# Performance work log

Hardware: AMD Instinct MI355X
Metric: run time of the kernel (lower is better)

## Reference

```python
import jax, jax.numpy as jnp
import numpy as np

N = 20000   # nodes
E = 320000  # edges (avg degree 16)
K = 3       # Chebyshev order


def _glorot(key, shape):
    fan_in, fan_out = shape[-2], shape[-1]
    lim = (6.0 / (fan_in + fan_out)) ** 0.5
    return jax.random.uniform(key, shape, minval=-lim, maxval=lim, dtype=jnp.float32)


def setup_inputs() -> dict:
    key = jax.random.key(0)
    ks = jax.random.split(key, 8)
    v = jax.random.normal(ks[0], (N, 86), dtype=jnp.float32)
    edges = jax.random.randint(ks[1], (2, E), 0, N, dtype=jnp.int32)
    W1 = _glorot(ks[2], (K, 86, 128));  b1 = jnp.zeros((128,), jnp.float32)
    W2 = _glorot(ks[3], (K, 128, 256)); b2 = jnp.zeros((256,), jnp.float32)
    W3 = _glorot(ks[4], (K, 256, 512)); b3 = jnp.zeros((512,), jnp.float32)
    return {"v": v, "edges": edges, "W1": W1, "b1": b1,
            "W2": W2, "b2": b2, "W3": W3, "b3": b3}


def _cheb_norm(edges, n):
    # PyG ChebConv with sym norm, lambda_max=2: L_hat = L - I = -D^-1/2 A D^-1/2
    # (diagonal entries from get_laplacian (+1) and add_self_loops (-1) cancel).
    # Self loops are removed before computing the Laplacian -> mask them out.
    row, col = edges[0], edges[1]
    w = (row != col).astype(jnp.float32)
    deg = jax.ops.segment_sum(w, row, num_segments=n)
    dinv = jnp.where(deg > 0, jax.lax.rsqrt(jnp.maximum(deg, 1e-12)), 0.0)
    norm_w = -dinv[row] * w * dinv[col]  # [E]
    return row, col, norm_w


def _cheb_conv(x, row, col, norm_w, W, b):
    # W: [K, in, out]
    def prop(z):  # L_hat @ z via edge gather + segment scatter-add
        return jax.ops.segment_sum(norm_w[:, None] * z[col], row, num_segments=x.shape[0])
    Tx0 = x
    out = Tx0 @ W[0]
    Tx1 = prop(Tx0)
    out = out + Tx1 @ W[1]
    Tx2 = 2.0 * prop(Tx1) - Tx0
    out = out + Tx2 @ W[2]
    return out + b


def reference(v, edges, W1, b1, W2, b2, W3, b3):
    row, col, norm_w = _cheb_norm(edges, v.shape[0])
    nk = jax.random.key(42)
    x1 = jax.nn.relu(_cheb_conv(v, row, col, norm_w, W1, b1))
    x1 = x1 * jax.random.normal(jax.random.fold_in(nk, 1), x1.shape, x1.dtype)
    x2 = jax.nn.relu(_cheb_conv(x1, row, col, norm_w, W2, b2))
    x2 = x2 * jax.random.normal(jax.random.fold_in(nk, 2), x2.shape, x2.dtype)
    x3 = jax.nn.relu(_cheb_conv(x2, row, col, norm_w, W3, b3))
    x3 = x3 * jax.random.normal(jax.random.fold_in(nk, 3), x3.shape, x3.dtype)
    return (x1, x2, x3)
```

## Files before the change

### kernel.cpp

```cpp
#include <hip/hip_runtime.h>
#include <stdint.h>
#include <math.h>

#define DEV static __device__ __forceinline__

typedef __attribute__((ext_vector_type(8))) short bf16x8;
typedef __attribute__((ext_vector_type(4))) float f32x4;
typedef __attribute__((ext_vector_type(8))) unsigned short u16x8;

DEV uint32_t rotl32(uint32_t v, int d) { return (v << d) | (v >> (32 - d)); }

DEV void threefry2x32(uint32_t k0, uint32_t k1, uint32_t& x0, uint32_t& x1) {
  const uint32_t k2 = k0 ^ k1 ^ 0x1BD11BDAu;
  x0 += k0; x1 += k1;
#define TFR(R) { x0 += x1; x1 = rotl32(x1, R) ^ x0; }
  TFR(13) TFR(15) TFR(26) TFR(6)
  x0 += k1; x1 += k2 + 1u;
  TFR(17) TFR(29) TFR(16) TFR(24)
  x0 += k2; x1 += k0 + 2u;
  TFR(13) TFR(15) TFR(26) TFR(6)
  x0 += k0; x1 += k1 + 3u;
  TFR(17) TFR(29) TFR(16) TFR(24)
  x0 += k1; x1 += k2 + 4u;
  TFR(13) TFR(15) TFR(26) TFR(6)
  x0 += k2; x1 += k0 + 5u;
#undef TFR
}

DEV float erfinv_f32(float x) {
  float w = -log1pf(-x * x);
  float p;
  if (w < 5.0f) {
    w -= 2.5f;
    p = 2.81022636e-08f;
    p = fmaf(p, w, 3.43273939e-07f);
    p = fmaf(p, w, -3.5233877e-06f);
    p = fmaf(p, w, -4.39150654e-06f);
    p = fmaf(p, w, 0.00021858087f);
    p = fmaf(p, w, -0.00125372503f);
    p = fmaf(p, w, -0.00417768164f);
    p = fmaf(p, w, 0.246640727f);
    p = fmaf(p, w, 1.50140941f);
  } else {
    w = sqrtf(w) - 3.0f;
    p = -0.000200214257f;
    p = fmaf(p, w, 0.000100950558f);
    p = fmaf(p, w, 0.00134934322f);
    p = fmaf(p, w, -0.00367342844f);
    p = fmaf(p, w, 0.00573950773f);
    p = fmaf(p, w, -0.0076224613f);
    p = fmaf(p, w, 0.00943887047f);
    p = fmaf(p, w, 1.00167406f);
    p = fmaf(p, w, 2.83297682f);
  }
  return p * x;
}

DEV float normal_from_bits(uint32_t bits) {
  float f = __uint_as_float((bits >> 9) | 0x3F800000u) - 1.0f;
  const float lo = -0.99999994f;
  float u = fmaf(f, 2.0f, lo);
  u = fmaxf(u, lo);
  return 1.41421356f * erfinv_f32(u);
}

DEV unsigned short f2bf(float f) {
  uint32_t u = __float_as_uint(f);
  uint32_t r = u + 0x7FFFu + ((u >> 16) & 1u);
  return (unsigned short)(r >> 16);
}

DEV float bf2f(uint32_t h) { return __uint_as_float(h << 16); }

__global__ void count_kernel(const int* __restrict__ rows, const int* __restrict__ cols,
                             int* __restrict__ counts, int* __restrict__ degs, int E) {
  int e = blockIdx.x * blockDim.x + threadIdx.x;
  if (e < E) {
    int r = rows[e];
    atomicAdd(&counts[r], 1);
    if (r != cols[e]) atomicAdd(&degs[r], 1);
  }
}

__global__ void dinv_kernel(const int* __restrict__ degs, float* __restrict__ dinv, int N) {
  int i = blockIdx.x * blockDim.x + threadIdx.x;
  if (i < N) {
    int d = degs[i];
    dinv[i] = d > 0 ? rsqrtf((float)d) : 0.0f;
  }
}

#define SCAN_T 1024
__global__ __launch_bounds__(SCAN_T) void scan_kernel(const int* __restrict__ counts,
                                                      int* __restrict__ row_ptr,
                                                      int* __restrict__ cursor, int N) {
  __shared__ int sa[SCAN_T], sb[SCAN_T];
  const int t = threadIdx.x;
  const int CH = (N + SCAN_T - 1) / SCAN_T;
  int base = t * CH;
  int psum = 0;
  for (int k = 0; k < CH; ++k) {
    int idx = base + k;
    if (idx < N) psum += counts[idx];
  }
  sa[t] = psum;
  __syncthreads();
  int* src = sa; int* dst = sb;
  for (int off = 1; off < SCAN_T; off <<= 1) {
    int v = src[t];
    if (t >= off) v += src[t - off];
    dst[t] = v;
    __syncthreads();
    int* tmp = src; src = dst; dst = tmp;
  }
  int running = src[t] - psum;
  for (int k = 0; k < CH; ++k) {
    int idx = base + k;
    if (idx < N) {
      row_ptr[idx] = running;
      cursor[idx] = running;
      running += counts[idx];
    }
  }
  if (t == SCAN_T - 1) row_ptr[N] = running;
}

__global__ void fill_kernel(const int* __restrict__ rows, const int* __restrict__ cols,
                            const float* __restrict__ dinv, int* __restrict__ cursor,
                            float2* __restrict__ ecv, int E) {
  int e = blockIdx.x * blockDim.x + threadIdx.x;
  if (e < E) {
    int r = rows[e], c = cols[e];
    float w = (r != c) ? -dinv[r] * dinv[c] : 0.0f;
    int pos = atomicAdd(&cursor[r], 1);
    ecv[pos] = make_float2(__int_as_float(c), w);
  }
}

template <int VEC>
DEV void ldrow(const unsigned short* base, size_t off, float* v) {
  const unsigned short* p = base + off;
  if (VEC == 4) {
    uint2 u = *(const uint2*)p;
    v[0] = bf2f(u.x & 0xffffu); v[1] = bf2f(u.x >> 16);
    v[2] = bf2f(u.y & 0xffffu); v[3] = bf2f(u.y >> 16);
  } else {
    uint32_t u = *(const uint32_t*)p;
    v[0] = bf2f(u & 0xffffu); v[1] = bf2f(u >> 16);
  }
}

template <int VEC, int SUB>
__global__ __launch_bounds__(256) void gather_prop(
    const int* __restrict__ row_ptr, const float2* __restrict__ ecv,
    const unsigned short* __restrict__ xsrc, int sstride,
    const float* __restrict__ xsub, int substride,
    unsigned short* __restrict__ outb, int N, int F, int Fpad) {
  const int wave = threadIdx.x >> 6, lane = threadIdx.x & 63;
  const int node = blockIdx.x * 4 + wave;
  if (node >= N) return;
  const int f0 = lane * VEC;
  if (f0 >= Fpad) return;
  const bool live = (f0 + VEC) <= F;
  float acc[VEC] = {};
  if (live) {
    const int s = row_ptr[node], e = row_ptr[node + 1];
    int j = s;
    for (; j + 8 <= e; j += 8) {
      float2 cw[8];
      float vv[8][VEC];
#pragma unroll
      for (int q = 0; q < 8; ++q) cw[q] = ecv[j + q];
#pragma unroll
      for (int q = 0; q < 8; ++q)
        ldrow<VEC>(xsrc, (size_t)__float_as_int(cw[q].x) * sstride + f0, vv[q]);
#pragma unroll
      for (int q = 0; q < 8; ++q)
#pragma unroll
        for (int z = 0; z < VEC; ++z) acc[z] = fmaf(cw[q].y, vv[q][z], acc[z]);
    }
    for (; j < e; ++j) {
      float2 cw = ecv[j];
      float vv[VEC];
      ldrow<VEC>(xsrc, (size_t)__float_as_int(cw.x) * sstride + f0, vv);
#pragma unroll
      for (int z = 0; z < VEC; ++z) acc[z] = fmaf(cw.y, vv[z], acc[z]);
    }
    if (SUB) {
      const float* sb = xsub + (size_t)node * substride + f0;
#pragma unroll
      for (int z = 0; z < VEC; ++z) acc[z] = fmaf(2.0f, acc[z], -sb[z]);
    }
  }
  size_t ob = (size_t)node * Fpad + f0;
  if (VEC == 4) {
    uint2 u;
    u.x = (uint32_t)f2bf(acc[0]) | ((uint32_t)f2bf(acc[1]) << 16);
    u.y = (uint32_t)f2bf(acc[2]) | ((uint32_t)f2bf(acc[3]) << 16);
    *(uint2*)&outb[ob] = u;
  } else {
    uint32_t u = (uint32_t)f2bf(acc[0]) | ((uint32_t)f2bf(acc[1]) << 16);
    *(uint32_t*)&outb[ob] = u;
  }
}

__global__ void wtrans_kernel(const float* __restrict__ W, unsigned short* __restrict__ Wt,
                              int F, int Fpad, int O) {
  int idx = blockIdx.x * 256 + threadIdx.x;
  int total = 3 * O * Fpad;
  if (idx >= total) return;
  int k = idx % Fpad;
  int o = (idx / Fpad) % O;
  int p = idx / (Fpad * O);
  Wt[idx] = (k < F) ? f2bf(W[((size_t)p * F + k) * O + o]) : (unsigned short)0;
}

__global__ void vconv_kernel(const float* __restrict__ v, unsigned short* __restrict__ vb, int N) {
  int i = blockIdx.x * 256 + threadIdx.x;
  if (i >= N * 96) return;
  int r = i / 96, k = i % 96;
  vb[i] = (k < 86) ? f2bf(v[(size_t)r * 86 + k]) : (unsigned short)0;
}

template <int BM, int FPAD, int KS>
__global__ __launch_bounds__(512, 4) void gemm3_db(
    const unsigned short* __restrict__ A0, const unsigned short* __restrict__ A1,
    const unsigned short* __restrict__ A2,
    const unsigned short* __restrict__ Wt, const float* __restrict__ bias,
    int M, int O, float* __restrict__ out, unsigned short* __restrict__ outb,
    int obstride, int fold) {
  constexpr int BN = 128;
  constexpr int NSP = FPAD / KS;
  constexpr int NSTEP = 3 * NSP;
  constexpr int CPR = KS / 8;
  constexpr int LST = KS + 8;
  constexpr int NA = BM * CPR;
  constexpr int NB = BN * CPR;
  constexpr int ACH = (NA + 511) / 512;
  constexpr int BCH = (NB + 511) / 512;
  constexpr int MFR = BM / 32;
  constexpr int KK = KS / 32;

  __shared__ unsigned short sA[2][BM * LST];
  __shared__ unsigned short sB[2][BN * LST];

  const int tid = threadIdx.x;
  const int lane = tid & 63;
  const int wave = tid >> 6;
  const int wm = wave >> 2, wo = wave & 3;
  const int bm = blockIdx.x * BM;
  const int bo = blockIdx.y * BN;
  const int l15 = lane & 15;
  const int kg = (lane >> 4) * 8;

  f32x4 acc[MFR][2] = {};
  const unsigned short* As[3] = {A0, A1, A2};

  u16x8 ra[ACH], rb[BCH];

  auto issue = [&](int s) {
    int p = s / NSP, k0 = (s % NSP) * KS;
    const unsigned short* __restrict__ A = As[p];
    const unsigned short* __restrict__ B = Wt + (size_t)p * O * FPAD;
#pragma unroll
    for (int c = 0; c < ACH; ++c) {
      int idx = tid + c * 512;
      if (NA % 512 == 0 || idx < NA) {
        int row = idx / CPR, ch = (idx % CPR) * 8;
        int gm = bm + row; if (gm >= M) gm = M - 1;
        ra[c] = *(const u16x8*)(A + (size_t)gm * FPAD + k0 + ch);
      }
    }
#pragma unroll
    for (int c = 0; c < BCH; ++c) {
      int idx = tid + c * 512;
      if (NB % 512 == 0 || idx < NB) {
        int row = idx / CPR, ch = (idx % CPR) * 8;
        rb[c] = *(const u16x8*)(B + (size_t)(bo + row) * FPAD + k0 + ch);
      }
    }
  };

  auto lds_write = [&](int buf) {
#pragma unroll
    for (int c = 0; c < ACH; ++c) {
      int idx = tid + c * 512;
      if (NA % 512 == 0 || idx < NA) {
        int row = idx / CPR, ch = (idx % CPR) * 8;
        *(u16x8*)&sA[buf][row * LST + ch] = ra[c];
      }
    }
#pragma unroll
    for (int c = 0; c < BCH; ++c) {
      int idx = tid + c * 512;
      if (NB % 512 == 0 || idx < NB) {
        int row = idx / CPR, ch = (idx % CPR) * 8;
        *(u16x8*)&sB[buf][row * LST + ch] = rb[c];
      }
    }
  };

  auto compute = [&](int buf) {
#pragma unroll
    for (int kk = 0; kk < KK; ++kk) {
      bf16x8 af[MFR], bfr[2];
#pragma unroll
      for (int mi = 0; mi < MFR; ++mi)
        af[mi] = *(const bf16x8*)&sA[buf][(wm * (BM / 2) + mi * 16 + l15) * LST + kk * 32 + kg];
#pragma unroll
      for (int ni = 0; ni < 2; ++ni)
        bfr[ni] = *(const bf16x8*)&sB[buf][(wo * 32 + ni * 16 + l15) * LST + kk * 32 + kg];
#pragma unroll
      for (int mi = 0; mi < MFR; ++mi)
#pragma unroll
        for (int ni = 0; ni < 2; ++ni)
          acc[mi][ni] = __builtin_amdgcn_mfma_f32_16x16x32_bf16(af[mi], bfr[ni], acc[mi][ni], 0, 0, 0);
    }
  };

  issue(0);
  lds_write(0);
  __syncthreads();

  int cur = 0;
#pragma unroll
  for (int s = 0; s < NSTEP; ++s) {
    if (s + 1 < NSTEP) issue(s + 1);
    compute(cur);
    if (s + 1 < NSTEP) {
      lds_write(cur ^ 1);
      __syncthreads();
      cur ^= 1;
    }
  }

  uint32_t f0 = 0u, f1 = (uint32_t)fold;
  threefry2x32(0u, 42u, f0, f1);
  const int r0 = (lane >> 4) * 4;
#pragma unroll
  for (int mi = 0; mi < MFR; ++mi) {
#pragma unroll
    for (int r = 0; r < 4; ++r) {
      int gm = bm + wm * (BM / 2) + mi * 16 + r0 + r;
      if (gm >= M) continue;
#pragma unroll
      for (int ni = 0; ni < 2; ++ni) {
        int go = bo + wo * 32 + ni * 16 + l15;
        float vv = acc[mi][ni][r] + bias[go];
        vv = vv > 0.0f ? vv : 0.0f;
        uint32_t a = 0u, b = (uint32_t)(gm * O + go);
        threefry2x32(f0, f1, a, b);
        float res = vv * normal_from_bits(a ^ b);
        out[(size_t)gm * O + go] = res;
        if (outb) outb[(size_t)gm * obstride + go] = f2bf(res);
      }
    }
  }
}

extern "C" void kernel_launch(void* const* d_in, const int* in_sizes, int n_in,
                              void* d_out, int out_size, void* d_ws, size_t ws_size,
                              hipStream_t stream) {
  const float* v    = (const float*)d_in[0];
  const int*  edges = (const int*)d_in[1];
  const float* W1 = (const float*)d_in[2];
  const float* b1 = (const float*)d_in[3];
  const float* W2 = (const float*)d_in[4];
  const float* b2 = (const float*)d_in[5];
  const float* W3 = (const float*)d_in[6];
  const float* b3 = (const float*)d_in[7];
  float* out = (float*)d_out;

  const int N = in_sizes[0] / 86;
  const int E = in_sizes[1] / 2;
  const int* rows = edges;
  const int* cols = edges + E;

  uintptr_t cur = (uintptr_t)d_ws;
  auto alloc = [&](size_t bytes) {
    cur = (cur + 15) & ~(uintptr_t)15;
    void* p = (void*)cur;
    cur += bytes;
    return p;
  };
  float2* ecv          = (float2*)alloc((size_t)E * 8);
  int* counts          = (int*)alloc((size_t)N * 4);
  int* degs            = (int*)alloc((size_t)N * 4);
  int* row_ptr         = (int*)alloc((size_t)(N + 1) * 4);
  int* cursor          = (int*)alloc((size_t)N * 4);
  float* dinv          = (float*)alloc((size_t)N * 4);
  unsigned short* tx1b = (unsigned short*)alloc((size_t)N * 256 * 2);
  unsigned short* tx2b = (unsigned short*)alloc((size_t)N * 256 * 2);
  unsigned short* vb   = (unsigned short*)alloc((size_t)N * 96 * 2);
  unsigned short* x1b  = (unsigned short*)alloc((size_t)N * 128 * 2);
  unsigned short* x2b  = (unsigned short*)alloc((size_t)N * 256 * 2);
  unsigned short* Wt   = (unsigned short*)alloc((size_t)3 * 512 * 256 * 2);

  float* x1 = out;
  float* x2 = x1 + (size_t)N * 128;
  float* x3 = x2 + (size_t)N * 256;

  hipMemsetAsync(counts, 0, (size_t)2 * N * sizeof(int), stream);
  count_kernel<<<(E + 255) / 256, 256, 0, stream>>>(rows, cols, counts, degs, E);
  dinv_kernel<<<(N + 255) / 256, 256, 0, stream>>>(degs, dinv, N);
  scan_kernel<<<1, SCAN_T, 0, stream>>>(counts, row_ptr, cursor, N);
  fill_kernel<<<(E + 255) / 256, 256, 0, stream>>>(rows, cols, dinv, cursor, ecv, E);
  vconv_kernel<<<(N * 96 + 255) / 256, 256, 0, stream>>>(v, vb, N);

  const int pblocks = (N + 3) / 4;

  {
    wtrans_kernel<<<(3 * 128 * 96 + 255) / 256, 256, 0, stream>>>(W1, Wt, 86, 96, 128);
    gather_prop<2, 0><<<pblocks, 256, 0, stream>>>(row_ptr, ecv, vb, 96, nullptr, 0, tx1b, N, 86, 96);
    gather_prop<2, 1><<<pblocks, 256, 0, stream>>>(row_ptr, ecv, tx1b, 96, v, 86, tx2b, N, 86, 96);
    dim3 g((N + 63) / 64, 1);
    gemm3_db<64, 96, 32><<<g, 512, 0, stream>>>(vb, tx1b, tx2b, Wt, b1, N, 128, x1, x1b, 128, 1);
  }
  {
    wtrans_kernel<<<(3 * 256 * 128 + 255) / 256, 256, 0, stream>>>(W2, Wt, 128, 128, 256);
    gather_prop<2, 0><<<pblocks, 256, 0, stream>>>(row_ptr, ecv, x1b, 128, nullptr, 0, tx1b, N, 128, 128);
    gather_prop<2, 1><<<pblocks, 256, 0, stream>>>(row_ptr, ecv, tx1b, 128, x1, 128, tx2b, N, 128, 128);
    dim3 g((N + 127) / 128, 2);
    gemm3_db<128, 128, 64><<<g, 512, 0, stream>>>(x1b, tx1b, tx2b, Wt, b2, N, 256, x2, x2b, 256, 2);
  }
  {
    wtrans_kernel<<<(3 * 512 * 256 + 255) / 256, 256, 0, stream>>>(W3, Wt, 256, 256, 512);
    gather_prop<4, 0><<<pblocks, 256, 0, stream>>>(row_ptr, ecv, x2b, 256, nullptr, 0, tx1b, N, 256, 256);
    gather_prop<4, 1><<<pblocks, 256, 0, stream>>>(row_ptr, ecv, tx1b, 256, x2, 256, tx2b, N, 256, 256);
    dim3 g((N + 127) / 128, 4);
    gemm3_db<128, 256, 64><<<g, 512, 0, stream>>>(x2b, tx1b, tx2b, Wt, b3, N, 512, x3, nullptr, 0, 3);
  }
}
```

Measured before the change: 408.0 us.

## Precompute dropout noise inside gather kernels and deepen GEMM register prefetch

Moves the threefry normal-noise generation out of the GEMM epilogue and into the memory-bound gather_prop kernels, which write it to a workspace buffer that the GEMM then reads. This overlaps ALU-heavy RNG with the latency-bound gather. The GEMM now prefetches global tiles two steps ahead using two register sets. The gather gains a 2-edge unrolled tail loop, and the dinv kernel is folded into fill_kernel. The trade-off is extra global traffic to write and read a noise buffer of up to N×512 floats, plus higher register pressure in the GEMM.

```diff
diff --git a/kernel.cpp b/kernel.cpp
--- a/kernel.cpp
+++ b/kernel.cpp
@@ -72,6 +72,16 @@
 
 DEV float bf2f(uint32_t h) { return __uint_as_float(h << 16); }
 
+DEV float4 noise4(uint32_t f0, uint32_t f1, uint32_t i4) {
+  uint32_t base = i4 * 4u;
+  float4 r;
+  { uint32_t a = 0u, b = base + 0u; threefry2x32(f0, f1, a, b); r.x = normal_from_bits(a ^ b); }
+  { uint32_t a = 0u, b = base + 1u; threefry2x32(f0, f1, a, b); r.y = normal_from_bits(a ^ b); }
+  { uint32_t a = 0u, b = base + 2u; threefry2x32(f0, f1, a, b); r.z = normal_from_bits(a ^ b); }
+  { uint32_t a = 0u, b = base + 3u; threefry2x32(f0, f1, a, b); r.w = normal_from_bits(a ^ b); }
+  return r;
+}
+
 __global__ void count_kernel(const int* __restrict__ rows, const int* __restrict__ cols,
                              int* __restrict__ counts, int* __restrict__ degs, int E) {
   int e = blockIdx.x * blockDim.x + threadIdx.x;
@@ -79,14 +89,6 @@
     int r = rows[e];
     atomicAdd(&counts[r], 1);
     if (r != cols[e]) atomicAdd(&degs[r], 1);
-  }
-}
-
-__global__ void dinv_kernel(const int* __restrict__ degs, float* __restrict__ dinv, int N) {
-  int i = blockIdx.x * blockDim.x + threadIdx.x;
-  if (i < N) {
-    int d = degs[i];
-    dinv[i] = d > 0 ? rsqrtf((float)d) : 0.0f;
   }
 }
 
@@ -126,12 +128,13 @@
 }
 
 __global__ void fill_kernel(const int* __restrict__ rows, const int* __restrict__ cols,
-                            const float* __restrict__ dinv, int* __restrict__ cursor,
+                            const int* __restrict__ degs, int* __restrict__ cursor,
                             float2* __restrict__ ecv, int E) {
   int e = blockIdx.x * blockDim.x + threadIdx.x;
   if (e < E) {
     int r = rows[e], c = cols[e];
-    float w = (r != c) ? -dinv[r] * dinv[c] : 0.0f;
+    int dr = degs[r], dc = degs[c];
+    float w = (r != c && dr > 0 && dc > 0) ? -rsqrtf((float)dr) * rsqrtf((float)dc) : 0.0f;
     int pos = atomicAdd(&cursor[r], 1);
     ecv[pos] = make_float2(__int_as_float(c), w);
   }
@@ -150,57 +153,78 @@
   }
 }
 
-template <int VEC, int SUB>
+template <int VEC, int SUB, int FOLD>
 __global__ __launch_bounds__(256) void gather_prop(
     const int* __restrict__ row_ptr, const float2* __restrict__ ecv,
     const unsigned short* __restrict__ xsrc, int sstride,
     const float* __restrict__ xsub, int substride,
-    unsigned short* __restrict__ outb, int N, int F, int Fpad) {
+    unsigned short* __restrict__ outb, int N, int F, int Fpad,
+    float* __restrict__ nbuf, int n4_begin, int n4_end) {
   const int wave = threadIdx.x >> 6, lane = threadIdx.x & 63;
   const int node = blockIdx.x * 4 + wave;
-  if (node >= N) return;
   const int f0 = lane * VEC;
-  if (f0 >= Fpad) return;
-  const bool live = (f0 + VEC) <= F;
-  float acc[VEC] = {};
-  if (live) {
-    const int s = row_ptr[node], e = row_ptr[node + 1];
-    int j = s;
-    for (; j + 8 <= e; j += 8) {
-      float2 cw[8];
-      float vv[8][VEC];
-#pragma unroll
-      for (int q = 0; q < 8; ++q) cw[q] = ecv[j + q];
-#pragma unroll
-      for (int q = 0; q < 8; ++q)
-        ldrow<VEC>(xsrc, (size_t)__float_as_int(cw[q].x) * sstride + f0, vv[q]);
-#pragma unroll
-      for (int q = 0; q < 8; ++q)
-#pragma unroll
-        for (int z = 0; z < VEC; ++z) acc[z] = fmaf(cw[q].y, vv[q][z], acc[z]);
-    }
-    for (; j < e; ++j) {
-      float2 cw = ecv[j];
-      float vv[VEC];
-      ldrow<VEC>(xsrc, (size_t)__float_as_int(cw.x) * sstride + f0, vv);
-#pragma unroll
-      for (int z = 0; z < VEC; ++z) acc[z] = fmaf(cw.y, vv[z], acc[z]);
-    }
-    if (SUB) {
-      const float* sb = xsub + (size_t)node * substride + f0;
-#pragma unroll
-      for (int z = 0; z < VEC; ++z) acc[z] = fmaf(2.0f, acc[z], -sb[z]);
-    }
-  }
-  size_t ob = (size_t)node * Fpad + f0;
-  if (VEC == 4) {
-    uint2 u;
-    u.x = (uint32_t)f2bf(acc[0]) | ((uint32_t)f2bf(acc[1]) << 16);
-    u.y = (uint32_t)f2bf(acc[2]) | ((uint32_t)f2bf(acc[3]) << 16);
-    *(uint2*)&outb[ob] = u;
-  } else {
-    uint32_t u = (uint32_t)f2bf(acc[0]) | ((uint32_t)f2bf(acc[1]) << 16);
-    *(uint32_t*)&outb[ob] = u;
+  if (node < N && f0 < Fpad) {
+    const bool live = (f0 + VEC) <= F;
+    float acc[VEC] = {};
+    if (live) {
+      const int s = row_ptr[node], e = row_ptr[node + 1];
+      int j = s;
+      for (; j + 8 <= e; j += 8) {
+        float2 cw[8];
+        float vv[8][VEC];
+#pragma unroll
+        for (int q = 0; q < 8; ++q) cw[q] = ecv[j + q];
+#pragma unroll
+        for (int q = 0; q < 8; ++q)
+          ldrow<VEC>(xsrc, (size_t)__float_as_int(cw[q].x) * sstride + f0, vv[q]);
+#pragma unroll
+        for (int q = 0; q < 8; ++q)
+#pragma unroll
+          for (int z = 0; z < VEC; ++z) acc[z] = fmaf(cw[q].y, vv[q][z], acc[z]);
+      }
+      for (; j + 2 <= e; j += 2) {
+        float2 cw[2];
+        float vv[2][VEC];
+#pragma unroll
+        for (int q = 0; q < 2; ++q) cw[q] = ecv[j + q];
+#pragma unroll
+        for (int q = 0; q < 2; ++q)
+          ldrow<VEC>(xsrc, (size_t)__float_as_int(cw[q].x) * sstride + f0, vv[q]);
+#pragma unroll
+        for (int q = 0; q < 2; ++q)
+#pragma unroll
+          for (int z = 0; z < VEC; ++z) acc[z] = fmaf(cw[q].y, vv[q][z], acc[z]);
+      }
+      for (; j < e; ++j) {
+        float2 cw = ecv[j];
+        float vv[VEC];
+        ldrow<VEC>(xsrc, (size_t)__float_as_int(cw.x) * sstride + f0, vv);
+#pragma unroll
+        for (int z = 0; z < VEC; ++z) acc[z] = fmaf(cw.y, vv[z], acc[z]);
+      }
+      if (SUB) {
+        const float* sb = xsub + (size_t)node * substride + f0;
+#pragma unroll
+        for (int z = 0; z < VEC; ++z) acc[z] = fmaf(2.0f, acc[z], -sb[z]);
+      }
+    }
+    size_t ob = (size_t)node * Fpad + f0;
+    if (VEC == 4) {
+      uint2 u;
+      u.x = (uint32_t)f2bf(acc[0]) | ((uint32_t)f2bf(acc[1]) << 16);
+      u.y = (uint32_t)f2bf(acc[2]) | ((uint32_t)f2bf(acc[3]) << 16);
+      *(uint2*)&outb[ob] = u;
+    } else {
+      uint32_t u = (uint32_t)f2bf(acc[0]) | ((uint32_t)f2bf(acc[1]) << 16);
+      *(uint32_t*)&outb[ob] = u;
+    }
+  }
+  uint32_t f0k = 0u, f1k = (uint32_t)FOLD;
+  threefry2x32(0u, 42u, f0k, f1k);
+  const int gstride = gridDim.x * 256;
+  for (int i4 = n4_begin + blockIdx.x * 256 + threadIdx.x; i4 < n4_end; i4 += gstride) {
+    float4 r = noise4(f0k, f1k, (uint32_t)i4);
+    *(float4*)&nbuf[(size_t)i4 * 4] = r;
   }
 }
 
@@ -227,8 +251,9 @@
     const unsigned short* __restrict__ A0, const unsigned short* __restrict__ A1,
     const unsigned short* __restrict__ A2,
     const unsigned short* __restrict__ Wt, const float* __restrict__ bias,
+    const float* __restrict__ noise,
     int M, int O, float* __restrict__ out, unsigned short* __restrict__ outb,
-    int obstride, int fold) {
+    int obstride) {
   constexpr int BN = 128;
   constexpr int NSP = FPAD / KS;
   constexpr int NSTEP = 3 * NSP;
@@ -256,9 +281,9 @@
   f32x4 acc[MFR][2] = {};
   const unsigned short* As[3] = {A0, A1, A2};
 
-  u16x8 ra[ACH], rb[BCH];
-
-  auto issue = [&](int s) {
+  u16x8 ra0[ACH], rb0[BCH], ra1[ACH], rb1[BCH];
+
+  auto issue = [&](int s, u16x8 (&ra)[ACH], u16x8 (&rb)[BCH]) {
     int p = s / NSP, k0 = (s % NSP) * KS;
     const unsigned short* __restrict__ A = As[p];
     const unsigned short* __restrict__ B = Wt + (size_t)p * O * FPAD;
@@ -281,7 +306,7 @@
     }
   };
 
-  auto lds_write = [&](int buf) {
+  auto lds_write = [&](int buf, u16x8 (&ra)[ACH], u16x8 (&rb)[BCH]) {
 #pragma unroll
     for (int c = 0; c < ACH; ++c) {
       int idx = tid + c * 512;
@@ -318,24 +343,24 @@
     }
   };
 
-  issue(0);
-  lds_write(0);
+  issue(0, ra0, rb0);
+  issue(1, ra1, rb1);
+  lds_write(0, ra0, rb0);
   __syncthreads();
 
-  int cur = 0;
 #pragma unroll
   for (int s = 0; s < NSTEP; ++s) {
-    if (s + 1 < NSTEP) issue(s + 1);
-    compute(cur);
-    if (s + 1 < NSTEP) {
-      lds_write(cur ^ 1);
-      __syncthreads();
-      cur ^= 1;
-    }
-  }
-
-  uint32_t f0 = 0u, f1 = (uint32_t)fold;
-  threefry2x32(0u, 42u, f0, f1);
+    if ((s & 1) == 0) {
+      if (s + 2 < NSTEP) issue(s + 2, ra0, rb0);
+      compute(s & 1);
+      if (s + 1 < NSTEP) { lds_write((s + 1) & 1, ra1, rb1); __syncthreads(); }
+    } else {
+      if (s + 2 < NSTEP) issue(s + 2, ra1, rb1);
+      compute(s & 1);
+      if (s + 1 < NSTEP) { lds_write((s + 1) & 1, ra0, rb0); __syncthreads(); }
+    }
+  }
+
   const int r0 = (lane >> 4) * 4;
 #pragma unroll
   for (int mi = 0; mi < MFR; ++mi) {
@@ -348,9 +373,7 @@
         int go = bo + wo * 32 + ni * 16 + l15;
         float vv = acc[mi][ni][r] + bias[go];
         vv = vv > 0.0f ? vv : 0.0f;
-        uint32_t a = 0u, b = (uint32_t)(gm * O + go);
-        threefry2x32(f0, f1, a, b);
-        float res = vv * normal_from_bits(a ^ b);
+        float res = vv * noise[(size_t)gm * O + go];
         out[(size_t)gm * O + go] = res;
         if (outb) outb[(size_t)gm * obstride + go] = f2bf(res);
       }
@@ -388,13 +411,13 @@
   int* degs            = (int*)alloc((size_t)N * 4);
   int* row_ptr         = (int*)alloc((size_t)(N + 1) * 4);
   int* cursor          = (int*)alloc((size_t)N * 4);
-  float* dinv          = (float*)alloc((size_t)N * 4);
   unsigned short* tx1b = (unsigned short*)alloc((size_t)N * 256 * 2);
   unsigned short* tx2b = (unsigned short*)alloc((size_t)N * 256 * 2);
   unsigned short* vb   = (unsigned short*)alloc((size_t)N * 96 * 2);
   unsigned short* x1b  = (unsigned short*)alloc((size_t)N * 128 * 2);
   unsigned short* x2b  = (unsigned short*)alloc((size_t)N * 256 * 2);
   unsigned short* Wt   = (unsigned short*)alloc((size_t)3 * 512 * 256 * 2);
+  float* nbuf          = (float*)alloc((size_t)N * 512 * 4);
 
   float* x1 = out;
   float* x2 = x1 + (size_t)N * 128;
@@ -402,32 +425,34 @@
 
   hipMemsetAsync(counts, 0, (size_t)2 * N * sizeof(int), stream);
   count_kernel<<<(E + 255) / 256, 256, 0, stream>>>(rows, cols, counts, degs, E);
-  dinv_kernel<<<(N + 255) / 256, 256, 0, stream>>>(degs, dinv, N);
   scan_kernel<<<1, SCAN_T, 0, stream>>>(counts, row_ptr, cursor, N);
-  fill_kernel<<<(E + 255) / 256, 256, 0, stream>>>(rows, cols, dinv, cursor, ecv, E);
+  fill_kernel<<<(E + 255) / 256, 256, 0, stream>>>(rows, cols, degs, cursor, ecv, E);
   vconv_kernel<<<(N * 96 + 255) / 256, 256, 0, stream>>>(v, vb, N);
 
   const int pblocks = (N + 3) / 4;
 
   {
     wtrans_kernel<<<(3 * 128 * 96 + 255) / 256, 256, 0, stream>>>(W1, Wt, 86, 96, 128);
-    gather_prop<2, 0><<<pblocks, 256, 0, stream>>>(row_ptr, ecv, vb, 96, nullptr, 0, tx1b, N, 86, 96);
-    gather_prop<2, 1><<<pblocks, 256, 0, stream>>>(row_ptr, ecv, tx1b, 96, v, 86, tx2b, N, 86, 96);
+    int t4 = N * 128 / 4, h4 = t4 / 2;
+    gather_prop<2, 0, 1><<<pblocks, 256, 0, stream>>>(row_ptr, ecv, vb, 96, nullptr, 0, tx1b, N, 86, 96, nbuf, 0, h4);
+    gather_prop<2, 1, 1><<<pblocks, 256, 0, stream>>>(row_ptr, ecv, tx1b, 96, v, 86, tx2b, N, 86, 96, nbuf, h4, t4);
     dim3 g((N + 63) / 64, 1);
-    gemm3_db<64, 96, 32><<<g, 512, 0, stream>>>(vb, tx1b, tx2b, Wt, b1, N, 128, x1, x1b, 128, 1);
+    gemm3_db<64, 96, 32><<<g, 512, 0, stream>>>(vb, tx1b, tx2b, Wt, b1, nbuf, N, 128, x1, x1b, 128);
   }
   {
     wtrans_kernel<<<(3 * 256 * 128 + 255) / 256, 256, 0, stream>>>(W2, Wt, 128, 128, 256);
-    gather_prop<2, 0><<<pblocks, 256, 0, stream>>>(row_ptr, ecv, x1b, 128, nullptr, 0, tx1b, N, 128, 128);
-    gather_prop<2, 1><<<pblocks, 256, 0, stream>>>(row_ptr, ecv, tx1b, 128, x1, 128, tx2b, N, 128, 128);
+    int t4 = N * 256 / 4, h4 = t4 / 2;
+    gather_prop<2, 0, 2><<<pblocks, 256, 0, stream>>>(row_ptr, ecv, x1b, 128, nullptr, 0, tx1b, N, 128, 128, nbuf, 0, h4);
+    gather_prop<2, 1, 2><<<pblocks, 256, 0, stream>>>(row_ptr, ecv, tx1b, 128, x1, 128, tx2b, N, 128, 128, nbuf, h4, t4);
     dim3 g((N + 127) / 128, 2);
-    gemm3_db<128, 128, 64><<<g, 512, 0, stream>>>(x1b, tx1b, tx2b, Wt, b2, N, 256, x2, x2b, 256, 2);
+    gemm3_db<128, 128, 64><<<g, 512, 0, stream>>>(x1b, tx1b, tx2b, Wt, b2, nbuf, N, 256, x2, x2b, 256);
   }
   {
     wtrans_kernel<<<(3 * 512 * 256 + 255) / 256, 256, 0, stream>>>(W3, Wt, 256, 256, 512);
-    gather_prop<4, 0><<<pblocks, 256, 0, stream>>>(row_ptr, ecv, x2b, 256, nullptr, 0, tx1b, N, 256, 256);
-    gather_prop<4, 1><<<pblocks, 256, 0, stream>>>(row_ptr, ecv, tx1b, 256, x2, 256, tx2b, N, 256, 256);
+    int t4 = N * 512 / 4, h4 = t4 / 2;
+    gather_prop<4, 0, 3><<<pblocks, 256, 0, stream>>>(row_ptr, ecv, x2b, 256, nullptr, 0, tx1b, N, 256, 256, nbuf, 0, h4);
+    gather_prop<4, 1, 3><<<pblocks, 256, 0, stream>>>(row_ptr, ecv, tx1b, 256, x2, 256, tx2b, N, 256, 256, nbuf, h4, t4);
     dim3 g((N + 127) / 128, 4);
-    gemm3_db<128, 256, 64><<<g, 512, 0, stream>>>(x2b, tx1b, tx2b, Wt, b3, N, 512, x3, nullptr, 0, 3);
-  }
-}
+    gemm3_db<128, 256, 64><<<g, 512, 0, stream>>>(x2b, tx1b, tx2b, Wt, b3, nbuf, N, 512, x3, nullptr, 0);
+  }
+}
```

Result: faster. 370.3 us (-9.2%).
